# Kernel tuning notes

Measured on AMD Instinct MI355X. Metric: run time of the kernel, lower is better.

## Reference

```python
import jax, jax.numpy as jnp
import numpy as np

N_PROMPT = 20
N_SAMPLES = 10000


def setup_inputs() -> dict:
    key = jax.random.key(0)
    k1, k2, k3, k4 = jax.random.split(key, 4)
    B, L, D = 32, 512, 768
    sample_id_tensor = jax.random.randint(k1, (B,), 0, N_SAMPLES, dtype=jnp.int64)
    input_embeds = jax.random.normal(k2, (B, L, D), dtype=jnp.float32)
    attention_mask = jax.random.randint(k3, (B, L), 0, 2, dtype=jnp.int32)
    # learned parameter: per-sample prompt embeddings, std=0.02 init
    prompt_embeddings = 0.02 * jax.random.normal(k4, (N_SAMPLES, N_PROMPT, D), dtype=jnp.float32)
    return {
        "sample_id_tensor": sample_id_tensor,
        "input_embeds": input_embeds,
        "attention_mask": attention_mask,
        "prompt_embeddings": prompt_embeddings,
    }


def reference(sample_id_tensor, input_embeds, attention_mask, prompt_embeddings):
    # sample_id_to_index is identity (sample_id_list = range(N_SAMPLES))
    prompts = prompt_embeddings[sample_id_tensor]            # [B, n_prompt, D]
    pad = attention_mask == 0                                # [B, L]
    # rank of each pad slot among pad slots of its row (0-based)
    rank = jnp.cumsum(pad.astype(jnp.int32), axis=1) - 1     # [B, L]
    take = pad & (rank < N_PROMPT)                           # first min(K, n_prompt) pads
    safe_rank = jnp.clip(rank, 0, N_PROMPT - 1)
    # gather prompt row `rank` for each position (only used where `take`)
    gathered = jnp.take_along_axis(prompts, safe_rank[:, :, None], axis=1)  # [B, L, D]
    inputs_embeds_new = jnp.where(take[:, :, None], gathered, input_embeds)
    attention_mask_new = jnp.where(take, jnp.ones_like(attention_mask), attention_mask)
    return (inputs_embeds_new, attention_mask_new)
```

## Files before the change

### kernel.cpp

```cpp
#include <hip/hip_runtime.h>
#include <hip/hip_bf16.h>

#define B_DIM 32
#define L_DIM 512
#define D_DIM 768
#define N_PROMPT 20
#define D4 (D_DIM / 4)
#define TOTAL4 (B_DIM * L_DIM * D4)

__global__ void prompt_scan_kernel(const int* __restrict__ mask,
                                   int* __restrict__ src,
                                   float* __restrict__ out_mask) {
    const int b = blockIdx.x;
    const int lane = threadIdx.x;
    int base = 0;
    const int row_off = b * L_DIM;
    for (int chunk = 0; chunk < L_DIM; chunk += 64) {
        const int l = chunk + lane;
        const int m = mask[row_off + l];
        const bool pad = (m == 0);
        const unsigned long long bal = __ballot(pad);
        const unsigned long long lower_mask =
            (lane == 0) ? 0ULL : (bal & ((1ULL << lane) - 1ULL));
        const int rank = base + __popcll(lower_mask);
        const bool take = pad && (rank < N_PROMPT);
        src[row_off + l] = take ? rank : -1;
        out_mask[row_off + l] = take ? 1.0f : (float)m;
        base += __popcll(bal);
    }
}

__global__ void prompt_copy_kernel(const float4* __restrict__ in_embeds,
                                   const float4* __restrict__ prompts,
                                   const int* __restrict__ sids,
                                   const int* __restrict__ src,
                                   float4* __restrict__ out) {
    int idx = blockIdx.x * blockDim.x + threadIdx.x;
    const int stride = gridDim.x * blockDim.x;
    for (; idx < TOTAL4; idx += stride) {
        const int pos = idx / D4;
        const int d = idx - pos * D4;
        const int s = src[pos];
        float4 v;
        if (s >= 0) {
            const int b = pos / L_DIM;
            const int sid = sids[b];
            v = prompts[((size_t)sid * N_PROMPT + s) * D4 + d];
        } else {
            v = in_embeds[idx];
        }
        out[idx] = v;
    }
}

extern "C" void kernel_launch(void* const* d_in, const int* in_sizes, int n_in,
                              void* d_out, int out_size, void* d_ws, size_t ws_size,
                              hipStream_t stream) {
    const int*   sids     = (const int*)d_in[0];
    const float* embeds   = (const float*)d_in[1];
    const int*   mask     = (const int*)d_in[2];
    const float* prompts  = (const float*)d_in[3];

    float* out_embeds = (float*)d_out;
    float* out_mask   = out_embeds + (size_t)B_DIM * L_DIM * D_DIM;

    int* src = (int*)d_ws;

    prompt_scan_kernel<<<B_DIM, 64, 0, stream>>>(mask, src, out_mask);

    const int block = 256;
    const int grid = (TOTAL4 + block - 1) / block;
    prompt_copy_kernel<<<grid, block, 0, stream>>>(
        (const float4*)embeds, (const float4*)prompts, sids, src,
        (float4*)out_embeds);
}
```

Measured before the change: 690.6 us.

## Fuse pad-rank scan and embedding copy into one sliced kernel

Replaces the separate scan and copy kernels with a single kernel. Each of 512 blocks recomputes its row's pad ranks in shared memory using a wave-ballot scan, then copies one slice of 32 positions. This removes a kernel launch, the workspace round trip, and the per-element global src lookup. In exchange the mask scan is repeated by all 16 slice blocks of a row, and the grid shrinks to 512 blocks of 256 threads, which may limit memory-level parallelism for a bandwidth-bound copy.

```diff
diff --git a/kernel.cpp b/kernel.cpp
--- a/kernel.cpp
+++ b/kernel.cpp
@@ -6,71 +6,89 @@
 #define D_DIM 768
 #define N_PROMPT 20
 #define D4 (D_DIM / 4)
-#define TOTAL4 (B_DIM * L_DIM * D4)
+#define SLICES 16
+#define L_PER_SLICE (L_DIM / SLICES)
 
-__global__ void prompt_scan_kernel(const int* __restrict__ mask,
-                                   int* __restrict__ src,
-                                   float* __restrict__ out_mask) {
-    const int b = blockIdx.x;
-    const int lane = threadIdx.x;
-    int base = 0;
+__global__ __launch_bounds__(256) void prompt_fused_kernel(
+    const int* __restrict__ sids,
+    const float4* __restrict__ embeds,
+    const int* __restrict__ mask,
+    const float4* __restrict__ prompts,
+    float4* __restrict__ out_embeds,
+    float* __restrict__ out_mask) {
+    const int b = blockIdx.x >> 4;
+    const int slice = blockIdx.x & (SLICES - 1);
+    const int tid = threadIdx.x;
+    const int lane = tid & 63;
+    const int wave = tid >> 6;
+
+    __shared__ short rank_s[L_DIM];
+    __shared__ int chunk_cnt[8];
+
     const int row_off = b * L_DIM;
-    for (int chunk = 0; chunk < L_DIM; chunk += 64) {
-        const int l = chunk + lane;
-        const int m = mask[row_off + l];
-        const bool pad = (m == 0);
-        const unsigned long long bal = __ballot(pad);
-        const unsigned long long lower_mask =
-            (lane == 0) ? 0ULL : (bal & ((1ULL << lane) - 1ULL));
-        const int rank = base + __popcll(lower_mask);
-        const bool take = pad && (rank < N_PROMPT);
-        src[row_off + l] = take ? rank : -1;
-        out_mask[row_off + l] = take ? 1.0f : (float)m;
-        base += __popcll(bal);
+
+    const int l0 = wave * 64 + lane;
+    const int l1 = 256 + wave * 64 + lane;
+    const int m0 = mask[row_off + l0];
+    const int m1 = mask[row_off + l1];
+    const unsigned long long bal0 = __ballot(m0 == 0);
+    const unsigned long long bal1 = __ballot(m1 == 0);
+    if (lane == 0) {
+        chunk_cnt[wave]     = __popcll(bal0);
+        chunk_cnt[wave + 4] = __popcll(bal1);
     }
-}
+    __syncthreads();
+    int base0 = 0, base1 = 0;
+    #pragma unroll
+    for (int j = 0; j < 8; ++j) {
+        const int c = chunk_cnt[j];
+        if (j < wave)     base0 += c;
+        if (j < wave + 4) base1 += c;
+    }
+    const unsigned long long lower = (1ULL << lane) - 1ULL;
+    const int r0 = base0 + __popcll(bal0 & lower);
+    const int r1 = base1 + __popcll(bal1 & lower);
+    const bool t0 = (m0 == 0) && (r0 < N_PROMPT);
+    const bool t1 = (m1 == 0) && (r1 < N_PROMPT);
+    rank_s[l0] = t0 ? (short)r0 : (short)-1;
+    rank_s[l1] = t1 ? (short)r1 : (short)-1;
+    if (slice == 0) {
+        out_mask[row_off + l0] = t0 ? 1.0f : (float)m0;
+        out_mask[row_off + l1] = t1 ? 1.0f : (float)m1;
+    }
+    __syncthreads();
 
-__global__ void prompt_copy_kernel(const float4* __restrict__ in_embeds,
-                                   const float4* __restrict__ prompts,
-                                   const int* __restrict__ sids,
-                                   const int* __restrict__ src,
-                                   float4* __restrict__ out) {
-    int idx = blockIdx.x * blockDim.x + threadIdx.x;
-    const int stride = gridDim.x * blockDim.x;
-    for (; idx < TOTAL4; idx += stride) {
-        const int pos = idx / D4;
-        const int d = idx - pos * D4;
-        const int s = src[pos];
+    const int sid = sids[b];
+    const int l_base = slice * L_PER_SLICE;
+    #pragma unroll 4
+    for (int i = tid; i < L_PER_SLICE * D4; i += 256) {
+        const int l_off = i / D4;
+        const int d = i - l_off * D4;
+        const int l = l_base + l_off;
+        const int s = rank_s[l];
+        const size_t out_idx = ((size_t)row_off + l) * (size_t)D4 + d;
         float4 v;
         if (s >= 0) {
-            const int b = pos / L_DIM;
-            const int sid = sids[b];
-            v = prompts[((size_t)sid * N_PROMPT + s) * D4 + d];
+            v = prompts[((size_t)sid * N_PROMPT + s) * (size_t)D4 + d];
         } else {
-            v = in_embeds[idx];
+            v = embeds[out_idx];
         }
-        out[idx] = v;
+        out_embeds[out_idx] = v;
     }
 }
 
 extern "C" void kernel_launch(void* const* d_in, const int* in_sizes, int n_in,
                               void* d_out, int out_size, void* d_ws, size_t ws_size,
                               hipStream_t stream) {
-    const int*   sids     = (const int*)d_in[0];
-    const float* embeds   = (const float*)d_in[1];
-    const int*   mask     = (const int*)d_in[2];
-    const float* prompts  = (const float*)d_in[3];
+    const int*   sids    = (const int*)d_in[0];
+    const float* embeds  = (const float*)d_in[1];
+    const int*   mask    = (const int*)d_in[2];
+    const float* prompts = (const float*)d_in[3];
 
     float* out_embeds = (float*)d_out;
     float* out_mask   = out_embeds + (size_t)B_DIM * L_DIM * D_DIM;
 
-    int* src = (int*)d_ws;
-
-    prompt_scan_kernel<<<B_DIM, 64, 0, stream>>>(mask, src, out_mask);
-
-    const int block = 256;
-    const int grid = (TOTAL4 + block - 1) / block;
-    prompt_copy_kernel<<<grid, block, 0, stream>>>(
-        (const float4*)embeds, (const float4*)prompts, sids, src,
-        (float4*)out_embeds);
+    prompt_fused_kernel<<<B_DIM * SLICES, 256, 0, stream>>>(
+        sids, (const float4*)embeds, mask, (const float4*)prompts,
+        (float4*)out_embeds, out_mask);
 }
```

Result: no change. 693.5 us (+0.4%).
